# Kernel tuning notes

Hardware: AMD Instinct MI355X
Metric: run time of the kernel (lower is better)

## Reference

```python
import jax, jax.numpy as jnp
import numpy as np

B, D_IN, H, D_OUT, K = 8192, 2048, 2048, 1024, 4
LOGVAR_INIT = -5.0


def setup_inputs() -> dict:
    key = jax.random.key(0)
    ks = jax.random.split(key, 32)
    dims = [(D_IN, H), (H, H), (H, D_OUT)]
    inp = {"x": jax.random.normal(ks[0], (B, D_IN), dtype=jnp.float32)}
    i = 1
    for l, (din, dout) in enumerate(dims):
        inp[f"w_mu{l}"] = 0.1 * jax.random.normal(ks[i], (K, dout, din), dtype=jnp.float32); i += 1
        inp[f"b_mu{l}"] = 0.1 * jax.random.normal(ks[i], (K, dout), dtype=jnp.float32); i += 1
        inp[f"w_lv{l}"] = jnp.full((K,), LOGVAR_INIT, dtype=jnp.float32)
        inp[f"b_lv{l}"] = jnp.full((K,), LOGVAR_INIT, dtype=jnp.float32)
        inp[f"ml{l}"] = jnp.zeros((K,), dtype=jnp.float32)
        # reparameterization noise (randn_like in the torch code), one per component
        inp[f"w_n{l}"] = jax.random.normal(ks[i], (K, dout, din), dtype=jnp.float32); i += 1
        inp[f"b_n{l}"] = jax.random.normal(ks[i], (K, dout), dtype=jnp.float32); i += 1
    return inp


def _mixture_linear(x, w_mu, b_mu, w_lv, b_lv, ml, w_n, b_n):
    # n_components <= n_samples: all K components used, weighted by softmax(mix_logits)
    mix_w = jax.nn.softmax(ml)                               # [K]
    w = w_mu + jnp.exp(0.5 * w_lv)[:, None, None] * w_n      # [K, O, I]
    b = b_mu + jnp.exp(0.5 * b_lv)[:, None] * b_n            # [K, O]
    # sum_k mix_w[k] * (x @ w[k].T + b[k])
    out = jnp.einsum('bi,koi,k->bo', x, w, mix_w)
    out = out + jnp.einsum('k,ko->o', mix_w, b)
    return out


def reference(x,
              w_mu0, b_mu0, w_lv0, b_lv0, ml0, w_n0, b_n0,
              w_mu1, b_mu1, w_lv1, b_lv1, ml1, w_n1, b_n1,
              w_mu2, b_mu2, w_lv2, b_lv2, ml2, w_n2, b_n2):
    h = jax.nn.relu(_mixture_linear(x, w_mu0, b_mu0, w_lv0, b_lv0, ml0, w_n0, b_n0))
    h = jax.nn.relu(_mixture_linear(h, w_mu1, b_mu1, w_lv1, b_lv1, ml1, w_n1, b_n1))
    h = _mixture_linear(h, w_mu2, b_mu2, w_lv2, b_lv2, ml2, w_n2, b_n2)
    return jax.nn.softmax(h, axis=1)
```

## Files before the change

### kernel.cpp

```cpp
#include <hip/hip_runtime.h>
#include <hip/hip_fp16.h>

typedef _Float16 half8 __attribute__((ext_vector_type(8)));
typedef _Float16 half4 __attribute__((ext_vector_type(4)));
typedef float floatx16 __attribute__((ext_vector_type(16)));

#define GLDS16(g, l)                                                           \
  __builtin_amdgcn_global_load_lds(                                            \
      (const __attribute__((address_space(1))) void*)(g),                      \
      (__attribute__((address_space(3))) void*)(l), 16, 0, 0)

__device__ inline void mix_coeffs(const float* lv, const float* ml,
                                  float* cmu, float* cn) {
  float m0 = ml[0], m1 = ml[1], m2 = ml[2], m3 = ml[3];
  float mx = fmaxf(fmaxf(m0, m1), fmaxf(m2, m3));
  float e0 = __expf(m0 - mx), e1 = __expf(m1 - mx);
  float e2 = __expf(m2 - mx), e3 = __expf(m3 - mx);
  float inv = 1.0f / (e0 + e1 + e2 + e3);
  cmu[0] = e0 * inv; cmu[1] = e1 * inv; cmu[2] = e2 * inv; cmu[3] = e3 * inv;
  cn[0] = cmu[0] * __expf(0.5f * lv[0]);
  cn[1] = cmu[1] * __expf(0.5f * lv[1]);
  cn[2] = cmu[2] * __expf(0.5f * lv[2]);
  cn[3] = cmu[3] * __expf(0.5f * lv[3]);
}

__device__ inline void do_prep_w(const float* __restrict__ mu,
                                 const float* __restrict__ nz,
                                 const float* lv, const float* ml,
                                 _Float16* __restrict__ out, int count,
                                 int bid) {
  float cmu[4], cn[4];
  mix_coeffs(lv, ml, cmu, cn);
  long i = ((long)bid * 256 + threadIdx.x) * 4;
  float rx = 0.f, ry = 0.f, rz = 0.f, rw = 0.f;
#pragma unroll
  for (int k = 0; k < 4; ++k) {
    float4 a = *(const float4*)(mu + (long)k * count + i);
    float4 b = *(const float4*)(nz + (long)k * count + i);
    rx += cmu[k] * a.x + cn[k] * b.x;
    ry += cmu[k] * a.y + cn[k] * b.y;
    rz += cmu[k] * a.z + cn[k] * b.z;
    rw += cmu[k] * a.w + cn[k] * b.w;
  }
  half4 h = {(_Float16)rx, (_Float16)ry, (_Float16)rz, (_Float16)rw};
  *(half4*)(out + i) = h;
}

__device__ inline void do_prep_b(const float* __restrict__ bmu,
                                 const float* __restrict__ bn,
                                 const float* lv, const float* ml,
                                 float* __restrict__ out, int O, int bid) {
  float cmu[4], cn[4];
  mix_coeffs(lv, ml, cmu, cn);
  int i = bid * 256 + threadIdx.x;
  if (i >= O) return;
  float r = 0.f;
#pragma unroll
  for (int k = 0; k < 4; ++k)
    r += cmu[k] * bmu[k * O + i] + cn[k] * bn[k * O + i];
  out[i] = r;
}

__device__ inline void do_cvt(const float* __restrict__ in,
                              _Float16* __restrict__ out, int bid) {
  long i = ((long)bid * 256 + threadIdx.x) * 4;
  float4 v = *(const float4*)(in + i);
  half4 h = {(_Float16)v.x, (_Float16)v.y, (_Float16)v.z, (_Float16)v.w};
  *(half4*)(out + i) = h;
}

struct PrepArgs {
  const float* x; _Float16* x16;
  const float* wmu0; const float* wn0; const float* wlv0; const float* ml0; _Float16* W0;
  const float* wmu1; const float* wn1; const float* wlv1; const float* ml1; _Float16* W1;
  const float* wmu2; const float* wn2; const float* wlv2; const float* ml2; _Float16* W2;
  const float* bmu0; const float* bn0; const float* blv0; float* b0;
  const float* bmu1; const float* bn1; const float* blv1; float* b1;
  const float* bmu2; const float* bn2; const float* blv2; float* b2;
};

__global__ __launch_bounds__(256) void prep_all(PrepArgs a) {
  int b = blockIdx.x;
  if (b < 16384) { do_cvt(a.x, a.x16, b); return; }
  b -= 16384;
  if (b < 4096) { do_prep_w(a.wmu0, a.wn0, a.wlv0, a.ml0, a.W0, 2048 * 2048, b); return; }
  b -= 4096;
  if (b < 4096) { do_prep_w(a.wmu1, a.wn1, a.wlv1, a.ml1, a.W1, 2048 * 2048, b); return; }
  b -= 4096;
  if (b < 2048) { do_prep_w(a.wmu2, a.wn2, a.wlv2, a.ml2, a.W2, 1024 * 2048, b); return; }
  b -= 2048;
  if (b < 8) { do_prep_b(a.bmu0, a.bn0, a.blv0, a.ml0, a.b0, 2048, b); return; }
  b -= 8;
  if (b < 8) { do_prep_b(a.bmu1, a.bn1, a.blv1, a.ml1, a.b1, 2048, b); return; }
  b -= 8;
  do_prep_b(a.bmu2, a.bn2, a.blv2, a.ml2, a.b2, 1024, b);
}

template <int CT, bool RELU, bool OUT_HALF>
__global__ __launch_bounds__(256, 2) void gemm_nt(
    const _Float16* __restrict__ A, const _Float16* __restrict__ B,
    const float* __restrict__ bias, void* __restrict__ Cout,
    int M, int N, int K) {
  constexpr int BN = CT * 64;
  __shared__ _Float16 sA[128 * 64];
  __shared__ _Float16 sB[BN * 64];

  const int t = threadIdx.x;
  const int l = t & 63;
  const int w = t >> 6;
  const int wr = w >> 1;
  const int wc = w & 1;
  const long rowBlock = (long)blockIdx.x * 128;
  const long colBlock = (long)blockIdx.y * BN;

  floatx16 acc[2][CT] = {};

  const _Float16* ga[4];
  const _Float16* gb[2 * CT];
#pragma unroll
  for (int j = 0; j < 4; ++j) {
    int p = j * 256 + t;
    int r = p >> 3, pos = p & 7;
    int gc = pos ^ (r & 7);
    ga[j] = A + (rowBlock + r) * (long)K + gc * 8;
  }
#pragma unroll
  for (int j = 0; j < 2 * CT; ++j) {
    int p = j * 256 + t;
    int r = p >> 3, pos = p & 7;
    int gc = pos ^ (r & 7);
    gb[j] = B + (colBlock + r) * (long)K + gc * 8;
  }
  char* stA = (char*)sA + w * 1024;
  char* stB = (char*)sB + w * 1024;

  const int rm = l & 31;
  const int kh = l >> 5;
  const int sw = rm & 7;

  for (int k0 = 0; k0 < K; k0 += 64) {
#pragma unroll
    for (int j = 0; j < 4; ++j) GLDS16(ga[j] + k0, stA + j * 4096);
#pragma unroll
    for (int j = 0; j < 2 * CT; ++j) GLDS16(gb[j] + k0, stB + j * 4096);
    __syncthreads();
#pragma unroll
    for (int s = 0; s < 4; ++s) {
      const int pos = (s * 2 + kh) ^ sw;
      half8 af[2], bf[CT];
#pragma unroll
      for (int rt = 0; rt < 2; ++rt)
        af[rt] = *(const half8*)((const char*)sA +
                                 ((wr * 64 + rt * 32 + rm) * 128 + pos * 16));
#pragma unroll
      for (int ct = 0; ct < CT; ++ct)
        bf[ct] = *(const half8*)((const char*)sB +
                                 ((wc * (CT * 32) + ct * 32 + rm) * 128 + pos * 16));
#pragma unroll
      for (int rt = 0; rt < 2; ++rt)
#pragma unroll
        for (int ct = 0; ct < CT; ++ct)
          acc[rt][ct] = __builtin_amdgcn_mfma_f32_32x32x16_f16(
              af[rt], bf[ct], acc[rt][ct], 0, 0, 0);
    }
    __syncthreads();
  }

  const int cl = l & 31;
  const int rh = (l >> 5) * 4;
#pragma unroll
  for (int rt = 0; rt < 2; ++rt) {
#pragma unroll
    for (int ct = 0; ct < CT; ++ct) {
      const long colg = colBlock + wc * (CT * 32) + ct * 32 + cl;
      const float bv = bias[colg];
#pragma unroll
      for (int reg = 0; reg < 16; ++reg) {
        const int rowin = (reg & 3) + 8 * (reg >> 2) + rh;
        const long rowg = rowBlock + wr * 64 + rt * 32 + rowin;
        float v = acc[rt][ct][reg] + bv;
        if (RELU) v = fmaxf(v, 0.0f);
        if (OUT_HALF)
          ((_Float16*)Cout)[rowg * N + colg] = (_Float16)v;
        else
          ((float*)Cout)[rowg * N + colg] = v;
      }
    }
  }
}

__global__ __launch_bounds__(256) void softmax_rows(float* __restrict__ io) {
  const int N = 1024;
  float* p = io + (long)blockIdx.x * N;
  int t = threadIdx.x;
  int w = t >> 6;
  float4 v = ((const float4*)p)[t];
  float m = fmaxf(fmaxf(v.x, v.y), fmaxf(v.z, v.w));
#pragma unroll
  for (int off = 32; off > 0; off >>= 1) m = fmaxf(m, __shfl_xor(m, off));
  __shared__ float red[8];
  if ((t & 63) == 0) red[w] = m;
  __syncthreads();
  m = fmaxf(fmaxf(red[0], red[1]), fmaxf(red[2], red[3]));
  float4 e;
  e.x = __expf(v.x - m); e.y = __expf(v.y - m);
  e.z = __expf(v.z - m); e.w = __expf(v.w - m);
  float s = e.x + e.y + e.z + e.w;
#pragma unroll
  for (int off = 32; off > 0; off >>= 1) s += __shfl_xor(s, off);
  if ((t & 63) == 0) red[4 + w] = s;
  __syncthreads();
  s = red[4] + red[5] + red[6] + red[7];
  float inv = 1.0f / s;
  float4 o = {e.x * inv, e.y * inv, e.z * inv, e.w * inv};
  ((float4*)p)[t] = o;
}

extern "C" void kernel_launch(void* const* d_in, const int* in_sizes, int n_in,
                              void* d_out, int out_size, void* d_ws,
                              size_t ws_size, hipStream_t stream) {
  char* ws = (char*)d_ws;
  _Float16* x16 = (_Float16*)(ws);
  _Float16* h0  = (_Float16*)(ws + 33554432);
  _Float16* W0  = (_Float16*)(ws + 67108864);
  _Float16* W1  = (_Float16*)(ws + 75497472);
  _Float16* W2  = (_Float16*)(ws + 83886080);
  float* b0 = (float*)(ws + 88080384);
  float* b1 = (float*)(ws + 88088576);
  float* b2 = (float*)(ws + 88096768);

  PrepArgs a;
  a.x = (const float*)d_in[0]; a.x16 = x16;
  a.wmu0 = (const float*)d_in[1];  a.bmu0 = (const float*)d_in[2];
  a.wlv0 = (const float*)d_in[3];  a.blv0 = (const float*)d_in[4];
  a.ml0  = (const float*)d_in[5];
  a.wn0  = (const float*)d_in[6];  a.bn0  = (const float*)d_in[7];
  a.wmu1 = (const float*)d_in[8];  a.bmu1 = (const float*)d_in[9];
  a.wlv1 = (const float*)d_in[10]; a.blv1 = (const float*)d_in[11];
  a.ml1  = (const float*)d_in[12];
  a.wn1  = (const float*)d_in[13]; a.bn1  = (const float*)d_in[14];
  a.wmu2 = (const float*)d_in[15]; a.bmu2 = (const float*)d_in[16];
  a.wlv2 = (const float*)d_in[17]; a.blv2 = (const float*)d_in[18];
  a.ml2  = (const float*)d_in[19];
  a.wn2  = (const float*)d_in[20]; a.bn2  = (const float*)d_in[21];
  a.W0 = W0; a.W1 = W1; a.W2 = W2; a.b0 = b0; a.b1 = b1; a.b2 = b2;

  prep_all<<<26644, 256, 0, stream>>>(a);

  gemm_nt<4, true, true><<<dim3(64, 8), 256, 0, stream>>>(
      x16, W0, b0, h0, 8192, 2048, 2048);
  gemm_nt<4, true, true><<<dim3(64, 8), 256, 0, stream>>>(
      h0, W1, b1, x16, 8192, 2048, 2048);
  gemm_nt<2, false, false><<<dim3(64, 8), 256, 0, stream>>>(
      x16, W2, b2, d_out, 8192, 1024, 2048);
  softmax_rows<<<8192, 256, 0, stream>>>((float*)d_out);
}
```

Before: 575.8 us.

## Double-buffer LDS in GEMM, enlarge tiles, and widen prep vectorization

Replaces the single-buffered GEMM with a templated version. The next K-slab is loaded into a second LDS buffer while MFMAs run on the current one, so each iteration needs one barrier instead of two. The two hidden-layer GEMMs move to 256x256 tiles with 8 waves, which raises data reuse per LDS load; the output GEMM uses 128x128 tiles. The prep kernel now handles 8 elements per thread with half8 stores, and the launch is reordered and shrunk to match. The big tiles use 128KB of LDS and 128 accumulator registers, so only one block fits per CU and the 256-block grid makes exactly one wave, which leaves little room to hide latency.

```diff
diff --git a/kernel.cpp b/kernel.cpp
--- a/kernel.cpp
+++ b/kernel.cpp
@@ -31,19 +31,44 @@
                                  int bid) {
   float cmu[4], cn[4];
   mix_coeffs(lv, ml, cmu, cn);
-  long i = ((long)bid * 256 + threadIdx.x) * 4;
-  float rx = 0.f, ry = 0.f, rz = 0.f, rw = 0.f;
-#pragma unroll
-  for (int k = 0; k < 4; ++k) {
-    float4 a = *(const float4*)(mu + (long)k * count + i);
-    float4 b = *(const float4*)(nz + (long)k * count + i);
-    rx += cmu[k] * a.x + cn[k] * b.x;
-    ry += cmu[k] * a.y + cn[k] * b.y;
-    rz += cmu[k] * a.z + cn[k] * b.z;
-    rw += cmu[k] * a.w + cn[k] * b.w;
-  }
-  half4 h = {(_Float16)rx, (_Float16)ry, (_Float16)rz, (_Float16)rw};
-  *(half4*)(out + i) = h;
+  long i = (long)bid * 2048 + threadIdx.x * 8;
+  float4 a0 = *(const float4*)(mu + 0L * count + i);
+  float4 a0b = *(const float4*)(mu + 0L * count + i + 4);
+  float4 a1 = *(const float4*)(mu + 1L * count + i);
+  float4 a1b = *(const float4*)(mu + 1L * count + i + 4);
+  float4 a2 = *(const float4*)(mu + 2L * count + i);
+  float4 a2b = *(const float4*)(mu + 2L * count + i + 4);
+  float4 a3 = *(const float4*)(mu + 3L * count + i);
+  float4 a3b = *(const float4*)(mu + 3L * count + i + 4);
+  float4 b0 = *(const float4*)(nz + 0L * count + i);
+  float4 b0b = *(const float4*)(nz + 0L * count + i + 4);
+  float4 b1 = *(const float4*)(nz + 1L * count + i);
+  float4 b1b = *(const float4*)(nz + 1L * count + i + 4);
+  float4 b2 = *(const float4*)(nz + 2L * count + i);
+  float4 b2b = *(const float4*)(nz + 2L * count + i + 4);
+  float4 b3 = *(const float4*)(nz + 3L * count + i);
+  float4 b3b = *(const float4*)(nz + 3L * count + i + 4);
+
+  float r0 = cmu[0]*a0.x + cn[0]*b0.x + cmu[1]*a1.x + cn[1]*b1.x
+           + cmu[2]*a2.x + cn[2]*b2.x + cmu[3]*a3.x + cn[3]*b3.x;
+  float r1 = cmu[0]*a0.y + cn[0]*b0.y + cmu[1]*a1.y + cn[1]*b1.y
+           + cmu[2]*a2.y + cn[2]*b2.y + cmu[3]*a3.y + cn[3]*b3.y;
+  float r2 = cmu[0]*a0.z + cn[0]*b0.z + cmu[1]*a1.z + cn[1]*b1.z
+           + cmu[2]*a2.z + cn[2]*b2.z + cmu[3]*a3.z + cn[3]*b3.z;
+  float r3 = cmu[0]*a0.w + cn[0]*b0.w + cmu[1]*a1.w + cn[1]*b1.w
+           + cmu[2]*a2.w + cn[2]*b2.w + cmu[3]*a3.w + cn[3]*b3.w;
+  float r4 = cmu[0]*a0b.x + cn[0]*b0b.x + cmu[1]*a1b.x + cn[1]*b1b.x
+           + cmu[2]*a2b.x + cn[2]*b2b.x + cmu[3]*a3b.x + cn[3]*b3b.x;
+  float r5 = cmu[0]*a0b.y + cn[0]*b0b.y + cmu[1]*a1b.y + cn[1]*b1b.y
+           + cmu[2]*a2b.y + cn[2]*b2b.y + cmu[3]*a3b.y + cn[3]*b3b.y;
+  float r6 = cmu[0]*a0b.z + cn[0]*b0b.z + cmu[1]*a1b.z + cn[1]*b1b.z
+           + cmu[2]*a2b.z + cn[2]*b2b.z + cmu[3]*a3b.z + cn[3]*b3b.z;
+  float r7 = cmu[0]*a0b.w + cn[0]*b0b.w + cmu[1]*a1b.w + cn[1]*b1b.w
+           + cmu[2]*a2b.w + cn[2]*b2b.w + cmu[3]*a3b.w + cn[3]*b3b.w;
+
+  half8 h = {(_Float16)r0, (_Float16)r1, (_Float16)r2, (_Float16)r3,
+             (_Float16)r4, (_Float16)r5, (_Float16)r6, (_Float16)r7};
+  *(half8*)(out + i) = h;
 }
 
 __device__ inline void do_prep_b(const float* __restrict__ bmu,
@@ -63,10 +88,12 @@
 
 __device__ inline void do_cvt(const float* __restrict__ in,
                               _Float16* __restrict__ out, int bid) {
-  long i = ((long)bid * 256 + threadIdx.x) * 4;
-  float4 v = *(const float4*)(in + i);
-  half4 h = {(_Float16)v.x, (_Float16)v.y, (_Float16)v.z, (_Float16)v.w};
-  *(half4*)(out + i) = h;
+  long i = (long)bid * 2048 + threadIdx.x * 8;
+  float4 v0 = *(const float4*)(in + i);
+  float4 v1 = *(const float4*)(in + i + 4);
+  half8 h = {(_Float16)v0.x, (_Float16)v0.y, (_Float16)v0.z, (_Float16)v0.w,
+             (_Float16)v1.x, (_Float16)v1.y, (_Float16)v1.z, (_Float16)v1.w};
+  *(half8*)(out + i) = h;
 }
 
 struct PrepArgs {
@@ -81,14 +108,14 @@
 
 __global__ __launch_bounds__(256) void prep_all(PrepArgs a) {
   int b = blockIdx.x;
-  if (b < 16384) { do_cvt(a.x, a.x16, b); return; }
-  b -= 16384;
-  if (b < 4096) { do_prep_w(a.wmu0, a.wn0, a.wlv0, a.ml0, a.W0, 2048 * 2048, b); return; }
-  b -= 4096;
-  if (b < 4096) { do_prep_w(a.wmu1, a.wn1, a.wlv1, a.ml1, a.W1, 2048 * 2048, b); return; }
-  b -= 4096;
-  if (b < 2048) { do_prep_w(a.wmu2, a.wn2, a.wlv2, a.ml2, a.W2, 1024 * 2048, b); return; }
+  if (b < 2048) { do_prep_w(a.wmu0, a.wn0, a.wlv0, a.ml0, a.W0, 2048 * 2048, b); return; }
   b -= 2048;
+  if (b < 2048) { do_prep_w(a.wmu1, a.wn1, a.wlv1, a.ml1, a.W1, 2048 * 2048, b); return; }
+  b -= 2048;
+  if (b < 1024) { do_prep_w(a.wmu2, a.wn2, a.wlv2, a.ml2, a.W2, 1024 * 2048, b); return; }
+  b -= 1024;
+  if (b < 8192) { do_cvt(a.x, a.x16, b); return; }
+  b -= 8192;
   if (b < 8) { do_prep_b(a.bmu0, a.bn0, a.blv0, a.ml0, a.b0, 2048, b); return; }
   b -= 8;
   if (b < 8) { do_prep_b(a.bmu1, a.bn1, a.blv1, a.ml1, a.b1, 2048, b); return; }
@@ -96,88 +123,108 @@
   do_prep_b(a.bmu2, a.bn2, a.blv2, a.ml2, a.b2, 1024, b);
 }
 
-template <int CT, bool RELU, bool OUT_HALF>
-__global__ __launch_bounds__(256, 2) void gemm_nt(
+template <int BM, int BN, int WM, int WN, bool RELU, bool OUT_HALF>
+__global__ __launch_bounds__((BM / WM) * (BN / WN) * 64, 2) void gemm2ph(
     const _Float16* __restrict__ A, const _Float16* __restrict__ B,
     const float* __restrict__ bias, void* __restrict__ Cout,
     int M, int N, int K) {
-  constexpr int BN = CT * 64;
-  __shared__ _Float16 sA[128 * 64];
-  __shared__ _Float16 sB[BN * 64];
+  constexpr int NWC = BN / WN;
+  constexpr int NWR = BM / WM;
+  constexpr int NW = NWC * NWR;
+  constexpr int NT = NW * 64;
+  constexpr int MT = WM / 32;
+  constexpr int CT = WN / 32;
+  constexpr int GA = BM * 8 / NT;
+  constexpr int GB = BN * 8 / NT;
+
+  __shared__ _Float16 sA[2][BM * 64];
+  __shared__ _Float16 sB[2][BN * 64];
 
   const int t = threadIdx.x;
   const int l = t & 63;
   const int w = t >> 6;
-  const int wr = w >> 1;
-  const int wc = w & 1;
-  const long rowBlock = (long)blockIdx.x * 128;
+  const int wr = w / NWC;
+  const int wc = w % NWC;
+  const long rowBlock = (long)blockIdx.x * BM;
   const long colBlock = (long)blockIdx.y * BN;
 
-  floatx16 acc[2][CT] = {};
-
-  const _Float16* ga[4];
-  const _Float16* gb[2 * CT];
-#pragma unroll
-  for (int j = 0; j < 4; ++j) {
-    int p = j * 256 + t;
+  floatx16 acc[MT][CT] = {};
+
+  const _Float16* ga[GA];
+  const _Float16* gb[GB];
+#pragma unroll
+  for (int j = 0; j < GA; ++j) {
+    int p = j * NT + t;
     int r = p >> 3, pos = p & 7;
     int gc = pos ^ (r & 7);
     ga[j] = A + (rowBlock + r) * (long)K + gc * 8;
   }
 #pragma unroll
-  for (int j = 0; j < 2 * CT; ++j) {
-    int p = j * 256 + t;
+  for (int j = 0; j < GB; ++j) {
+    int p = j * NT + t;
     int r = p >> 3, pos = p & 7;
     int gc = pos ^ (r & 7);
     gb[j] = B + (colBlock + r) * (long)K + gc * 8;
   }
-  char* stA = (char*)sA + w * 1024;
-  char* stB = (char*)sB + w * 1024;
 
   const int rm = l & 31;
   const int kh = l >> 5;
   const int sw = rm & 7;
 
+#pragma unroll
+  for (int j = 0; j < GA; ++j)
+    GLDS16(ga[j], (char*)sA[0] + w * 1024 + j * (NT * 16));
+#pragma unroll
+  for (int j = 0; j < GB; ++j)
+    GLDS16(gb[j], (char*)sB[0] + w * 1024 + j * (NT * 16));
+  __syncthreads();
+
+  int cur = 0;
   for (int k0 = 0; k0 < K; k0 += 64) {
-#pragma unroll
-    for (int j = 0; j < 4; ++j) GLDS16(ga[j] + k0, stA + j * 4096);
-#pragma unroll
-    for (int j = 0; j < 2 * CT; ++j) GLDS16(gb[j] + k0, stB + j * 4096);
-    __syncthreads();
+    if (k0 + 64 < K) {
+      const int nxt = cur ^ 1;
+#pragma unroll
+      for (int j = 0; j < GA; ++j)
+        GLDS16(ga[j] + k0 + 64, (char*)sA[nxt] + w * 1024 + j * (NT * 16));
+#pragma unroll
+      for (int j = 0; j < GB; ++j)
+        GLDS16(gb[j] + k0 + 64, (char*)sB[nxt] + w * 1024 + j * (NT * 16));
+    }
 #pragma unroll
     for (int s = 0; s < 4; ++s) {
       const int pos = (s * 2 + kh) ^ sw;
-      half8 af[2], bf[CT];
-#pragma unroll
-      for (int rt = 0; rt < 2; ++rt)
-        af[rt] = *(const half8*)((const char*)sA +
-                                 ((wr * 64 + rt * 32 + rm) * 128 + pos * 16));
+      half8 af[MT], bf[CT];
+#pragma unroll
+      for (int rt = 0; rt < MT; ++rt)
+        af[rt] = *(const half8*)((const char*)sA[cur] +
+                                 ((wr * WM + rt * 32 + rm) * 128 + pos * 16));
 #pragma unroll
       for (int ct = 0; ct < CT; ++ct)
-        bf[ct] = *(const half8*)((const char*)sB +
-                                 ((wc * (CT * 32) + ct * 32 + rm) * 128 + pos * 16));
-#pragma unroll
-      for (int rt = 0; rt < 2; ++rt)
+        bf[ct] = *(const half8*)((const char*)sB[cur] +
+                                 ((wc * WN + ct * 32 + rm) * 128 + pos * 16));
+#pragma unroll
+      for (int rt = 0; rt < MT; ++rt)
 #pragma unroll
         for (int ct = 0; ct < CT; ++ct)
           acc[rt][ct] = __builtin_amdgcn_mfma_f32_32x32x16_f16(
               af[rt], bf[ct], acc[rt][ct], 0, 0, 0);
     }
     __syncthreads();
+    cur ^= 1;
   }
 
   const int cl = l & 31;
   const int rh = (l >> 5) * 4;
 #pragma unroll
-  for (int rt = 0; rt < 2; ++rt) {
+  for (int rt = 0; rt < MT; ++rt) {
 #pragma unroll
     for (int ct = 0; ct < CT; ++ct) {
-      const long colg = colBlock + wc * (CT * 32) + ct * 32 + cl;
+      const long colg = colBlock + wc * WN + ct * 32 + cl;
       const float bv = bias[colg];
 #pragma unroll
       for (int reg = 0; reg < 16; ++reg) {
         const int rowin = (reg & 3) + 8 * (reg >> 2) + rh;
-        const long rowg = rowBlock + wr * 64 + rt * 32 + rowin;
+        const long rowg = rowBlock + wr * WM + rt * 32 + rowin;
         float v = acc[rt][ct][reg] + bv;
         if (RELU) v = fmaxf(v, 0.0f);
         if (OUT_HALF)
@@ -245,13 +292,13 @@
   a.wn2  = (const float*)d_in[20]; a.bn2  = (const float*)d_in[21];
   a.W0 = W0; a.W1 = W1; a.W2 = W2; a.b0 = b0; a.b1 = b1; a.b2 = b2;
 
-  prep_all<<<26644, 256, 0, stream>>>(a);
-
-  gemm_nt<4, true, true><<<dim3(64, 8), 256, 0, stream>>>(
+  prep_all<<<13332, 256, 0, stream>>>(a);
+
+  gemm2ph<256, 256, 128, 64, true, true><<<dim3(32, 8), 512, 0, stream>>>(
       x16, W0, b0, h0, 8192, 2048, 2048);
-  gemm_nt<4, true, true><<<dim3(64, 8), 256, 0, stream>>>(
+  gemm2ph<256, 256, 128, 64, true, true><<<dim3(32, 8), 512, 0, stream>>>(
       h0, W1, b1, x16, 8192, 2048, 2048);
-  gemm_nt<2, false, false><<<dim3(64, 8), 256, 0, stream>>>(
+  gemm2ph<128, 128, 64, 64, false, false><<<dim3(64, 8), 256, 0, stream>>>(
       x16, W2, b2, d_out, 8192, 1024, 2048);
   softmax_rows<<<8192, 256, 0, stream>>>((float*)d_out);
 }
```

Result: no change. 585.4 us (+1.7%).

## Use uniform 128x128 GEMM tiles with column-major grid and persistent prep kernel

Applied to the files above, without the earlier changes.

The GEMM kernel now always uses a 128x128 output tile instead of 128x256 (or 128x128 for the last layer). It swaps grid axes so consecutive blocks walk along N for the same A row block, and raises occupancy to 3 blocks per SM. The prep kernel becomes a grid-stride loop over 2048 blocks, with weight mixing ordered first and all eight loads issued up front. Smaller tiles lower register pressure and add more blocks for scheduling, but they reduce data reuse per tile and increase global and LDS traffic per FLOP.

```diff
diff --git a/kernel.cpp b/kernel.cpp
--- a/kernel.cpp
+++ b/kernel.cpp
@@ -27,23 +27,31 @@
 __device__ inline void do_prep_w(const float* __restrict__ mu,
                                  const float* __restrict__ nz,
                                  const float* lv, const float* ml,
-                                 _Float16* __restrict__ out, int count,
+                                 _Float16* __restrict__ out, long count4,
                                  int bid) {
   float cmu[4], cn[4];
   mix_coeffs(lv, ml, cmu, cn);
-  long i = ((long)bid * 256 + threadIdx.x) * 4;
-  float rx = 0.f, ry = 0.f, rz = 0.f, rw = 0.f;
-#pragma unroll
-  for (int k = 0; k < 4; ++k) {
-    float4 a = *(const float4*)(mu + (long)k * count + i);
-    float4 b = *(const float4*)(nz + (long)k * count + i);
-    rx += cmu[k] * a.x + cn[k] * b.x;
-    ry += cmu[k] * a.y + cn[k] * b.y;
-    rz += cmu[k] * a.z + cn[k] * b.z;
-    rw += cmu[k] * a.w + cn[k] * b.w;
-  }
+  long i = (long)bid * 256 + threadIdx.x;
+  const float4* m4 = (const float4*)mu;
+  const float4* n4 = (const float4*)nz;
+  float4 a0 = m4[0 * count4 + i];
+  float4 a1 = m4[1 * count4 + i];
+  float4 a2 = m4[2 * count4 + i];
+  float4 a3 = m4[3 * count4 + i];
+  float4 b0 = n4[0 * count4 + i];
+  float4 b1 = n4[1 * count4 + i];
+  float4 b2 = n4[2 * count4 + i];
+  float4 b3 = n4[3 * count4 + i];
+  float rx = cmu[0]*a0.x + cn[0]*b0.x + cmu[1]*a1.x + cn[1]*b1.x
+           + cmu[2]*a2.x + cn[2]*b2.x + cmu[3]*a3.x + cn[3]*b3.x;
+  float ry = cmu[0]*a0.y + cn[0]*b0.y + cmu[1]*a1.y + cn[1]*b1.y
+           + cmu[2]*a2.y + cn[2]*b2.y + cmu[3]*a3.y + cn[3]*b3.y;
+  float rz = cmu[0]*a0.z + cn[0]*b0.z + cmu[1]*a1.z + cn[1]*b1.z
+           + cmu[2]*a2.z + cn[2]*b2.z + cmu[3]*a3.z + cn[3]*b3.z;
+  float rw = cmu[0]*a0.w + cn[0]*b0.w + cmu[1]*a1.w + cn[1]*b1.w
+           + cmu[2]*a2.w + cn[2]*b2.w + cmu[3]*a3.w + cn[3]*b3.w;
   half4 h = {(_Float16)rx, (_Float16)ry, (_Float16)rz, (_Float16)rw};
-  *(half4*)(out + i) = h;
+  *(half4*)(out + i * 4) = h;
 }
 
 __device__ inline void do_prep_b(const float* __restrict__ bmu,
@@ -80,55 +88,51 @@
 };
 
 __global__ __launch_bounds__(256) void prep_all(PrepArgs a) {
-  int b = blockIdx.x;
-  if (b < 16384) { do_cvt(a.x, a.x16, b); return; }
-  b -= 16384;
-  if (b < 4096) { do_prep_w(a.wmu0, a.wn0, a.wlv0, a.ml0, a.W0, 2048 * 2048, b); return; }
-  b -= 4096;
-  if (b < 4096) { do_prep_w(a.wmu1, a.wn1, a.wlv1, a.ml1, a.W1, 2048 * 2048, b); return; }
-  b -= 4096;
-  if (b < 2048) { do_prep_w(a.wmu2, a.wn2, a.wlv2, a.ml2, a.W2, 1024 * 2048, b); return; }
-  b -= 2048;
-  if (b < 8) { do_prep_b(a.bmu0, a.bn0, a.blv0, a.ml0, a.b0, 2048, b); return; }
-  b -= 8;
-  if (b < 8) { do_prep_b(a.bmu1, a.bn1, a.blv1, a.ml1, a.b1, 2048, b); return; }
-  b -= 8;
-  do_prep_b(a.bmu2, a.bn2, a.blv2, a.ml2, a.b2, 1024, b);
-}
-
-template <int CT, bool RELU, bool OUT_HALF>
-__global__ __launch_bounds__(256, 2) void gemm_nt(
+  for (int wb = blockIdx.x; wb < 26644; wb += 2048) {
+    if (wb < 4096) {
+      do_prep_w(a.wmu0, a.wn0, a.wlv0, a.ml0, a.W0, 1048576, wb);
+    } else if (wb < 8192) {
+      do_prep_w(a.wmu1, a.wn1, a.wlv1, a.ml1, a.W1, 1048576, wb - 4096);
+    } else if (wb < 10240) {
+      do_prep_w(a.wmu2, a.wn2, a.wlv2, a.ml2, a.W2, 524288, wb - 8192);
+    } else if (wb < 26624) {
+      do_cvt(a.x, a.x16, wb - 10240);
+    } else if (wb < 26632) {
+      do_prep_b(a.bmu0, a.bn0, a.blv0, a.ml0, a.b0, 2048, wb - 26624);
+    } else if (wb < 26640) {
+      do_prep_b(a.bmu1, a.bn1, a.blv1, a.ml1, a.b1, 2048, wb - 26632);
+    } else {
+      do_prep_b(a.bmu2, a.bn2, a.blv2, a.ml2, a.b2, 1024, wb - 26640);
+    }
+  }
+}
+
+template <bool RELU, bool OUT_HALF>
+__global__ __launch_bounds__(256, 3) void gemm_nt(
     const _Float16* __restrict__ A, const _Float16* __restrict__ B,
     const float* __restrict__ bias, void* __restrict__ Cout,
     int M, int N, int K) {
-  constexpr int BN = CT * 64;
   __shared__ _Float16 sA[128 * 64];
-  __shared__ _Float16 sB[BN * 64];
+  __shared__ _Float16 sB[128 * 64];
 
   const int t = threadIdx.x;
   const int l = t & 63;
   const int w = t >> 6;
   const int wr = w >> 1;
   const int wc = w & 1;
-  const long rowBlock = (long)blockIdx.x * 128;
-  const long colBlock = (long)blockIdx.y * BN;
-
-  floatx16 acc[2][CT] = {};
+  const long rowBlock = (long)blockIdx.y * 128;
+  const long colBlock = (long)blockIdx.x * 128;
+
+  floatx16 acc[2][2] = {};
 
   const _Float16* ga[4];
-  const _Float16* gb[2 * CT];
+  const _Float16* gb[4];
 #pragma unroll
   for (int j = 0; j < 4; ++j) {
     int p = j * 256 + t;
     int r = p >> 3, pos = p & 7;
     int gc = pos ^ (r & 7);
     ga[j] = A + (rowBlock + r) * (long)K + gc * 8;
-  }
-#pragma unroll
-  for (int j = 0; j < 2 * CT; ++j) {
-    int p = j * 256 + t;
-    int r = p >> 3, pos = p & 7;
-    int gc = pos ^ (r & 7);
     gb[j] = B + (colBlock + r) * (long)K + gc * 8;
   }
   char* stA = (char*)sA + w * 1024;
@@ -142,24 +146,24 @@
 #pragma unroll
     for (int j = 0; j < 4; ++j) GLDS16(ga[j] + k0, stA + j * 4096);
 #pragma unroll
-    for (int j = 0; j < 2 * CT; ++j) GLDS16(gb[j] + k0, stB + j * 4096);
+    for (int j = 0; j < 4; ++j) GLDS16(gb[j] + k0, stB + j * 4096);
     __syncthreads();
 #pragma unroll
     for (int s = 0; s < 4; ++s) {
       const int pos = (s * 2 + kh) ^ sw;
-      half8 af[2], bf[CT];
+      half8 af[2], bf[2];
 #pragma unroll
       for (int rt = 0; rt < 2; ++rt)
         af[rt] = *(const half8*)((const char*)sA +
                                  ((wr * 64 + rt * 32 + rm) * 128 + pos * 16));
 #pragma unroll
-      for (int ct = 0; ct < CT; ++ct)
+      for (int ct = 0; ct < 2; ++ct)
         bf[ct] = *(const half8*)((const char*)sB +
-                                 ((wc * (CT * 32) + ct * 32 + rm) * 128 + pos * 16));
+                                 ((wc * 64 + ct * 32 + rm) * 128 + pos * 16));
 #pragma unroll
       for (int rt = 0; rt < 2; ++rt)
 #pragma unroll
-        for (int ct = 0; ct < CT; ++ct)
+        for (int ct = 0; ct < 2; ++ct)
           acc[rt][ct] = __builtin_amdgcn_mfma_f32_32x32x16_f16(
               af[rt], bf[ct], acc[rt][ct], 0, 0, 0);
     }
@@ -171,8 +175,8 @@
 #pragma unroll
   for (int rt = 0; rt < 2; ++rt) {
 #pragma unroll
-    for (int ct = 0; ct < CT; ++ct) {
-      const long colg = colBlock + wc * (CT * 32) + ct * 32 + cl;
+    for (int ct = 0; ct < 2; ++ct) {
+      const long colg = colBlock + wc * 64 + ct * 32 + cl;
       const float bv = bias[colg];
 #pragma unroll
       for (int reg = 0; reg < 16; ++reg) {
@@ -245,13 +249,13 @@
   a.wn2  = (const float*)d_in[20]; a.bn2  = (const float*)d_in[21];
   a.W0 = W0; a.W1 = W1; a.W2 = W2; a.b0 = b0; a.b1 = b1; a.b2 = b2;
 
-  prep_all<<<26644, 256, 0, stream>>>(a);
-
-  gemm_nt<4, true, true><<<dim3(64, 8), 256, 0, stream>>>(
+  prep_all<<<2048, 256, 0, stream>>>(a);
+
+  gemm_nt<true, true><<<dim3(16, 64), 256, 0, stream>>>(
       x16, W0, b0, h0, 8192, 2048, 2048);
-  gemm_nt<4, true, true><<<dim3(64, 8), 256, 0, stream>>>(
+  gemm_nt<true, true><<<dim3(16, 64), 256, 0, stream>>>(
       h0, W1, b1, x16, 8192, 2048, 2048);
-  gemm_nt<2, false, false><<<dim3(64, 8), 256, 0, stream>>>(
+  gemm_nt<false, false><<<dim3(8, 64), 256, 0, stream>>>(
       x16, W2, b2, d_out, 8192, 1024, 2048);
   softmax_rows<<<8192, 256, 0, stream>>>((float*)d_out);
 }
```

Result: slower. 617.8 us (+7.3%).
